# Optimization experiments

Measured on AMD Instinct MI355X. Metric: run time of the kernel, lower is better.

## Reference

```python
import jax, jax.numpy as jnp
import numpy as np

THRESHOLD = 0.7

def _ternize_ste(w, threshold):
    # delta computed without gradient (torch.no_grad in original)
    delta = jax.lax.stop_gradient(threshold * jnp.mean(jnp.abs(w)))
    ternary = jnp.where(w > delta, 1.0, jnp.where(w < -delta, -1.0, 0.0)).astype(w.dtype)
    # STE: forward value = ternary, backward gradient = identity w.r.t. w
    return ternary + (w - jax.lax.stop_gradient(w))

def setup_inputs() -> dict:
    key = jax.random.key(0)
    k1, k2 = jax.random.split(key)
    B, IN, OUT = 32, 4096, 11008
    x = jax.random.normal(k1, (B, IN), dtype=jnp.float32)
    # xavier_uniform init: U(-a, a), a = sqrt(6/(fan_in+fan_out))
    a = float(np.sqrt(6.0 / (IN + OUT)))
    weight = jax.random.uniform(k2, (OUT, IN), dtype=jnp.float32, minval=-a, maxval=a)
    alpha = jnp.ones((1,), dtype=jnp.float32)
    bias = jnp.zeros((OUT,), dtype=jnp.float32)
    return {"x": x, "weight": weight, "alpha": alpha, "bias": bias}

def reference(x, weight, alpha, bias):
    w_ternary = _ternize_ste(weight, THRESHOLD)  # [OUT, IN] values in {-1,0,1}*STE
    # F.linear(x, W*alpha, b) = x @ (W*alpha).T + b
    return jnp.einsum('bi,oi->bo', x, w_ternary * alpha[0]) + bias
```

## Files before the change

### kernel.cpp

```cpp
#include <hip/hip_runtime.h>
#include <hip/hip_bf16.h>

#define OUTN 11008
#define KDIM 4096
#define BDIM 32
#define NT16 688
#define WCOUNT 45088768
#define PF   8
#define NPB  1024

typedef __bf16 bf16x8 __attribute__((ext_vector_type(8)));
typedef float f32x4  __attribute__((ext_vector_type(4)));
typedef float f32x16 __attribute__((ext_vector_type(16)));

__device__ __forceinline__ ushort f2bf(float f) {
    unsigned u = __builtin_bit_cast(unsigned, f);
    u = (u + 0x7FFFu + ((u >> 16) & 1u)) >> 16;
    return (ushort)u;
}

__device__ __forceinline__ unsigned tern1(float w, float d) {
    unsigned b = __builtin_bit_cast(unsigned, w);
    unsigned s = (b & 0x80000000u) | 0x3F800000u;
    return (__builtin_fabsf(w) > d) ? s : 0u;
}
__device__ __forceinline__ unsigned ternpack(float a, float b, float d) {
    return __builtin_amdgcn_perm(tern1(b, d), tern1(a, d), 0x07060302u);
}

__device__ __forceinline__ float delta_fix(double delta_d) {
    float dc = (float)delta_d;
    if ((double)dc > delta_d)
        dc = __builtin_bit_cast(float, __builtin_bit_cast(unsigned, dc) - 1u);
    return dc;
}

__global__ __launch_bounds__(256) void prep_k(const float4* __restrict__ w4,
                                              const float* __restrict__ x,
                                              ushort* __restrict__ xb,
                                              double* __restrict__ dpart) {
    const int tid = blockIdx.x * 256 + threadIdx.x;

    if (threadIdx.x < 32) {
        const int i4 = blockIdx.x * 32 + threadIdx.x;
        const int elem = i4 * 4;
        const int b = elem >> 12;
        const int k = elem & (KDIM - 1);
        const float4 v = ((const float4*)x)[i4];
        ushort4 o;
        o.x = f2bf(v.x); o.y = f2bf(v.y); o.z = f2bf(v.z); o.w = f2bf(v.w);
        *(ushort4*)(xb + ((k >> 3) * 32 + b) * 8 + (k & 7)) = o;
    }

    double s = 0.0;
#pragma unroll 8
    for (int j = 0; j < 43; ++j) {
        float4 v = w4[tid + j * 262144];
        s += (double)(fabsf(v.x) + fabsf(v.y)) + (double)(fabsf(v.z) + fabsf(v.w));
    }
    for (int off = 32; off; off >>= 1) s += __shfl_down(s, off);
    __shared__ double red[4];
    const int lane = threadIdx.x & 63, wv = threadIdx.x >> 6;
    if (lane == 0) red[wv] = s;
    __syncthreads();
    if (threadIdx.x == 0) dpart[blockIdx.x] = red[0] + red[1] + red[2] + red[3];
}

__global__ __launch_bounds__(256, 3) void gemm16_k(const float* __restrict__ W,
                                                   const ushort* __restrict__ xb,
                                                   const double* __restrict__ dpart,
                                                   const float* __restrict__ alpha,
                                                   const float* __restrict__ bias,
                                                   float* __restrict__ out) {
    __shared__ float redf[3][32][16];
    __shared__ double redd[4];
    const int tid = threadIdx.x;
    const int wv = tid >> 6, l = tid & 63;

    {
        double s = 0.0;
#pragma unroll
        for (int j = 0; j < 4; ++j) s += dpart[tid * 4 + j];
        for (int off = 32; off; off >>= 1) s += __shfl_down(s, off);
        if ((tid & 63) == 0) redd[wv] = s;
    }
    __syncthreads();
    const double dsum = redd[0] + redd[1] + redd[2] + redd[3];
    const float delta = delta_fix(0.7 * dsum * (1.0 / (double)WCOUNT));

    const int o0 = blockIdx.x * 16;
    const int kw0 = wv * 1024;
    const int col = l & 15;
    const int kb  = l >> 4;

    const float4* wp = (const float4*)(W + (size_t)(o0 + col) * KDIM + kw0 + kb * 8);
    const uint4* xa0 = (const uint4*)xb + ((size_t)(kw0 >> 3) + kb) * 32 + col;
    const uint4* xa1 = xa0 + 16;

    f32x4 acc0, acc1;
#pragma unroll
    for (int i = 0; i < 4; ++i) { acc0[i] = 0.0f; acc1[i] = 0.0f; }

    float4 Wa[PF], Wb[PF];
    uint4  X0[PF], X1[PF];
#pragma unroll
    for (int p = 0; p < PF; ++p) {
        Wa[p] = wp[p * 8];
        Wb[p] = wp[p * 8 + 1];
        X0[p] = xa0[(size_t)p * 128];
        X1[p] = xa1[(size_t)p * 128];
    }
#pragma unroll
    for (int s = 0; s < 32; ++s) {
        const int bi = s & (PF - 1);
        uint4 bb;
        bb.x = ternpack(Wa[bi].x, Wa[bi].y, delta);
        bb.y = ternpack(Wa[bi].z, Wa[bi].w, delta);
        bb.z = ternpack(Wb[bi].x, Wb[bi].y, delta);
        bb.w = ternpack(Wb[bi].z, Wb[bi].w, delta);
        const bf16x8 bv = __builtin_bit_cast(bf16x8, bb);
        acc0 = __builtin_amdgcn_mfma_f32_16x16x32_bf16(
                   __builtin_bit_cast(bf16x8, X0[bi]), bv, acc0, 0, 0, 0);
        acc1 = __builtin_amdgcn_mfma_f32_16x16x32_bf16(
                   __builtin_bit_cast(bf16x8, X1[bi]), bv, acc1, 0, 0, 0);
        if (s + PF < 32) {
            Wa[bi] = wp[(s + PF) * 8];
            Wb[bi] = wp[(s + PF) * 8 + 1];
            X0[bi] = xa0[(size_t)(s + PF) * 128];
            X1[bi] = xa1[(size_t)(s + PF) * 128];
        }
    }

    if (wv > 0) {
#pragma unroll
        for (int j = 0; j < 4; ++j) {
            redf[wv - 1][kb * 4 + j][col]      = acc0[j];
            redf[wv - 1][16 + kb * 4 + j][col] = acc1[j];
        }
    }
    __syncthreads();
    if (wv == 0) {
        const float a = *alpha;
        const float bn = bias[o0 + col];
#pragma unroll
        for (int j = 0; j < 4; ++j) {
            const int m0 = kb * 4 + j;
            float v0 = acc0[j] + redf[0][m0][col] + redf[1][m0][col] + redf[2][m0][col];
            out[(size_t)m0 * OUTN + o0 + col] = fmaf(a, v0, bn);
            const int m1 = 16 + kb * 4 + j;
            float v1 = acc1[j] + redf[0][m1][col] + redf[1][m1][col] + redf[2][m1][col];
            out[(size_t)m1 * OUTN + o0 + col] = fmaf(a, v1, bn);
        }
    }
}

__global__ __launch_bounds__(256) void abssum_k(const float4* __restrict__ w4,
                                                double* __restrict__ dsum) {
    const int tid = blockIdx.x * 256 + threadIdx.x;
    double s = 0.0;
#pragma unroll 8
    for (int j = 0; j < 43; ++j) {
        float4 v = w4[tid + j * 262144];
        s += (double)(fabsf(v.x) + fabsf(v.y)) + (double)(fabsf(v.z) + fabsf(v.w));
    }
    for (int off = 32; off; off >>= 1) s += __shfl_down(s, off);
    __shared__ double red[4];
    const int lane = threadIdx.x & 63, wv = threadIdx.x >> 6;
    if (lane == 0) red[wv] = s;
    __syncthreads();
    if (threadIdx.x == 0) atomicAdd(dsum, red[0] + red[1] + red[2] + red[3]);
}

__global__ __launch_bounds__(64) void gemm1_k(const float* __restrict__ W,
                                              const float* __restrict__ x,
                                              const double* __restrict__ dsum,
                                              float* __restrict__ dst,
                                              const float* __restrict__ alpha,
                                              const float* __restrict__ bias) {
    const int l = threadIdx.x;
    const int o0 = blockIdx.x * 32;
    const float delta = delta_fix(0.7 * (*dsum) * (1.0 / (double)WCOUNT));
    const int row = l & 31, half = l >> 5;
    const float4* wp = (const float4*)(W + (size_t)(o0 + row) * KDIM + half * 8);
    const float4* xp = (const float4*)(x + (size_t)row * KDIM + half * 8);

    f32x16 acc;
#pragma unroll
    for (int i = 0; i < 16; ++i) acc[i] = 0.0f;

#pragma unroll 8
    for (int s = 0; s < 256; ++s) {
        float4 w0 = wp[s * 4], w1 = wp[s * 4 + 1];
        uint4 bb;
        bb.x = ternpack(w0.x, w0.y, delta);
        bb.y = ternpack(w0.z, w0.w, delta);
        bb.z = ternpack(w1.x, w1.y, delta);
        bb.w = ternpack(w1.z, w1.w, delta);
        float4 v0 = xp[s * 4], v1 = xp[s * 4 + 1];
        struct U { ushort s[8]; } uu;
        uu.s[0] = f2bf(v0.x); uu.s[1] = f2bf(v0.y);
        uu.s[2] = f2bf(v0.z); uu.s[3] = f2bf(v0.w);
        uu.s[4] = f2bf(v1.x); uu.s[5] = f2bf(v1.y);
        uu.s[6] = f2bf(v1.z); uu.s[7] = f2bf(v1.w);
        acc = __builtin_amdgcn_mfma_f32_32x32x16_bf16(
                  __builtin_bit_cast(bf16x8, uu), __builtin_bit_cast(bf16x8, bb),
                  acc, 0, 0, 0);
    }
    const float a = *alpha;
#pragma unroll
    for (int rg = 0; rg < 16; ++rg) {
        const int m = (rg & 3) + 8 * (rg >> 2) + 4 * half;
        const int n = o0 + row;
        dst[(size_t)m * OUTN + n] = fmaf(a, acc[rg], bias[n]);
    }
}

extern "C" void kernel_launch(void* const* d_in, const int* in_sizes, int n_in,
                              void* d_out, int out_size, void* d_ws, size_t ws_size,
                              hipStream_t stream) {
    const float* x     = (const float*)d_in[0];
    const float* W     = (const float*)d_in[1];
    const float* alpha = (const float*)d_in[2];
    const float* bias  = (const float*)d_in[3];
    float* out = (float*)d_out;

    const size_t PART_SZ = (size_t)NPB * 8;
    const size_t XBF_OFF = 65536;
    const size_t XBF_SZ  = (size_t)BDIM * KDIM * 2;

    if (ws_size >= XBF_OFF + XBF_SZ) {
        double* dpart = (double*)d_ws;
        ushort* xb = (ushort*)((char*)d_ws + XBF_OFF);
        prep_k<<<NPB, 256, 0, stream>>>((const float4*)W, x, xb, dpart);
        gemm16_k<<<NT16, 256, 0, stream>>>(W, xb, dpart, alpha, bias, out);
    } else {
        double* dsum = (double*)d_ws;
        (void)hipMemsetAsync(d_ws, 0, 16, stream);
        abssum_k<<<1024, 256, 0, stream>>>((const float4*)W, dsum);
        gemm1_k<<<344, 64, 0, stream>>>(W, x, dsum, out, alpha, bias);
    }
}
```

Measured before the change: 64.31 us.

## Precompute 2-bit ternary weight codes in the abs-sum pass, with a near-threshold exception list

The abs-sum pass that already streams all of W now also writes a 2-bit ternary code per weight. It uses a fixed threshold window placed around the expected delta, and weights inside that window are logged into a per-row exception list through atomics. The GEMM then reads the compact codes instead of re-reading the fp32 weights, which removes the second full pass over W. It fixes the ambiguous entries with a small fp32 correction using a transposed copy of x. If the computed delta falls outside the window, or a row overflows its exception list, it falls back to the original path. The window constants are tuned to the expected weight distribution, and the change adds atomics, extra workspace and a memset.

```diff
diff --git a/kernel.cpp b/kernel.cpp
--- a/kernel.cpp
+++ b/kernel.cpp
@@ -8,6 +8,8 @@
 #define WCOUNT 45088768
 #define PF   8
 #define NPB  1024
+#define DLO  0.0069400f
+#define DHI  0.0070115f
 
 typedef __bf16 bf16x8 __attribute__((ext_vector_type(8)));
 typedef float f32x4  __attribute__((ext_vector_type(4)));
@@ -35,9 +37,21 @@
     return dc;
 }
 
+__device__ __forceinline__ unsigned dec2(unsigned c, int j) {
+    unsigned c0 = (c >> (4 * j)) & 3u;
+    unsigned c1 = (c >> (4 * j + 2)) & 3u;
+    unsigned m = c0 | (c1 << 16);
+    unsigned sel = m + (m << 8) + 0x04000400u;
+    return __builtin_amdgcn_perm(0x00BF3F00u, 0x00808000u, sel);
+}
+
 __global__ __launch_bounds__(256) void prep_k(const float4* __restrict__ w4,
                                               const float* __restrict__ x,
                                               ushort* __restrict__ xb,
+                                              float* __restrict__ xT,
+                                              unsigned char* __restrict__ codes,
+                                              unsigned* __restrict__ cnt,
+                                              uint2* __restrict__ ebuf,
                                               double* __restrict__ dpart) {
     const int tid = blockIdx.x * 256 + threadIdx.x;
 
@@ -50,13 +64,41 @@
         ushort4 o;
         o.x = f2bf(v.x); o.y = f2bf(v.y); o.z = f2bf(v.z); o.w = f2bf(v.w);
         *(ushort4*)(xb + ((k >> 3) * 32 + b) * 8 + (k & 7)) = o;
+        xT[(size_t)(k + 0) * 32 + b] = v.x;
+        xT[(size_t)(k + 1) * 32 + b] = v.y;
+        xT[(size_t)(k + 2) * 32 + b] = v.z;
+        xT[(size_t)(k + 3) * 32 + b] = v.w;
     }
 
     double s = 0.0;
-#pragma unroll 8
+#pragma unroll 4
     for (int j = 0; j < 43; ++j) {
-        float4 v = w4[tid + j * 262144];
-        s += (double)(fabsf(v.x) + fabsf(v.y)) + (double)(fabsf(v.z) + fabsf(v.w));
+        const int i4 = tid + j * 262144;
+        const float4 v = w4[i4];
+        const int row = i4 >> 10;
+        const int kbase = (i4 & 1023) << 2;
+        unsigned cc[4];
+        const float e[4] = {v.x, v.y, v.z, v.w};
+#pragma unroll
+        for (int q = 0; q < 4; ++q) {
+            const float w = e[q];
+            const unsigned wb = __builtin_bit_cast(unsigned, w);
+            const float aw = __builtin_fabsf(w);
+            s += (double)aw;
+            unsigned c;
+            if (aw > DHI) {
+                c = 1u + (wb >> 31);
+            } else if (aw > DLO) {
+                c = 3u;
+                unsigned idx = atomicAdd(&cnt[row], 1u);
+                if (idx < 64u)
+                    ebuf[(size_t)row * 64 + idx] = make_uint2((unsigned)(kbase + q), wb);
+            } else {
+                c = 0u;
+            }
+            cc[q] = c;
+        }
+        codes[i4] = (unsigned char)(cc[0] | (cc[1] << 2) | (cc[2] << 4) | (cc[3] << 6));
     }
     for (int off = 32; off; off >>= 1) s += __shfl_down(s, off);
     __shared__ double red[4];
@@ -67,15 +109,22 @@
 }
 
 __global__ __launch_bounds__(256, 3) void gemm16_k(const float* __restrict__ W,
+                                                   const unsigned char* __restrict__ codes,
                                                    const ushort* __restrict__ xb,
+                                                   const float* __restrict__ xT,
+                                                   const uint2* __restrict__ ebuf,
+                                                   const unsigned* __restrict__ cnt,
                                                    const double* __restrict__ dpart,
                                                    const float* __restrict__ alpha,
                                                    const float* __restrict__ bias,
                                                    float* __restrict__ out) {
     __shared__ float redf[3][32][16];
+    __shared__ float corr[16][33];
     __shared__ double redd[4];
+    __shared__ int sbad;
     const int tid = threadIdx.x;
     const int wv = tid >> 6, l = tid & 63;
+    const int o0 = blockIdx.x * 16;
 
     {
         double s = 0.0;
@@ -84,16 +133,18 @@
         for (int off = 32; off; off >>= 1) s += __shfl_down(s, off);
         if ((tid & 63) == 0) redd[wv] = s;
     }
+    if (tid == 0) sbad = 0;
     __syncthreads();
     const double dsum = redd[0] + redd[1] + redd[2] + redd[3];
-    const float delta = delta_fix(0.7 * dsum * (1.0 / (double)WCOUNT));
-
-    const int o0 = blockIdx.x * 16;
+    const float dc = delta_fix(0.7 * dsum * (1.0 / (double)WCOUNT));
+    if (tid < 16 && cnt[o0 + tid] > 64u) sbad = 1;
+    __syncthreads();
+    const bool ok = (dc >= DLO) && (dc <= DHI) && (sbad == 0);
+
     const int kw0 = wv * 1024;
     const int col = l & 15;
     const int kb  = l >> 4;
 
-    const float4* wp = (const float4*)(W + (size_t)(o0 + col) * KDIM + kw0 + kb * 8);
     const uint4* xa0 = (const uint4*)xb + ((size_t)(kw0 >> 3) + kb) * 32 + col;
     const uint4* xa1 = xa0 + 16;
 
@@ -101,33 +152,49 @@
 #pragma unroll
     for (int i = 0; i < 4; ++i) { acc0[i] = 0.0f; acc1[i] = 0.0f; }
 
-    float4 Wa[PF], Wb[PF];
-    uint4  X0[PF], X1[PF];
-#pragma unroll
-    for (int p = 0; p < PF; ++p) {
-        Wa[p] = wp[p * 8];
-        Wb[p] = wp[p * 8 + 1];
-        X0[p] = xa0[(size_t)p * 128];
-        X1[p] = xa1[(size_t)p * 128];
-    }
-#pragma unroll
-    for (int s = 0; s < 32; ++s) {
-        const int bi = s & (PF - 1);
-        uint4 bb;
-        bb.x = ternpack(Wa[bi].x, Wa[bi].y, delta);
-        bb.y = ternpack(Wa[bi].z, Wa[bi].w, delta);
-        bb.z = ternpack(Wb[bi].x, Wb[bi].y, delta);
-        bb.w = ternpack(Wb[bi].z, Wb[bi].w, delta);
-        const bf16x8 bv = __builtin_bit_cast(bf16x8, bb);
-        acc0 = __builtin_amdgcn_mfma_f32_16x16x32_bf16(
-                   __builtin_bit_cast(bf16x8, X0[bi]), bv, acc0, 0, 0, 0);
-        acc1 = __builtin_amdgcn_mfma_f32_16x16x32_bf16(
-                   __builtin_bit_cast(bf16x8, X1[bi]), bv, acc1, 0, 0, 0);
-        if (s + PF < 32) {
-            Wa[bi] = wp[(s + PF) * 8];
-            Wb[bi] = wp[(s + PF) * 8 + 1];
-            X0[bi] = xa0[(size_t)(s + PF) * 128];
-            X1[bi] = xa1[(size_t)(s + PF) * 128];
+    if (ok) {
+        const ushort* cp = (const ushort*)codes + (size_t)(o0 + col) * 512 + (kw0 >> 3) + kb;
+        unsigned Cc[PF]; uint4 X0[PF], X1[PF];
+#pragma unroll
+        for (int p = 0; p < PF; ++p) {
+            Cc[p] = cp[p * 4];
+            X0[p] = xa0[(size_t)p * 128];
+            X1[p] = xa1[(size_t)p * 128];
+        }
+#pragma unroll
+        for (int s = 0; s < 32; ++s) {
+            const int bi = s & (PF - 1);
+            const unsigned c = Cc[bi];
+            uint4 bb;
+            bb.x = dec2(c, 0); bb.y = dec2(c, 1);
+            bb.z = dec2(c, 2); bb.w = dec2(c, 3);
+            const bf16x8 bv = __builtin_bit_cast(bf16x8, bb);
+            acc0 = __builtin_amdgcn_mfma_f32_16x16x32_bf16(
+                       __builtin_bit_cast(bf16x8, X0[bi]), bv, acc0, 0, 0, 0);
+            acc1 = __builtin_amdgcn_mfma_f32_16x16x32_bf16(
+                       __builtin_bit_cast(bf16x8, X1[bi]), bv, acc1, 0, 0, 0);
+            if (s + PF < 32) {
+                Cc[bi] = cp[(s + PF) * 4];
+                X0[bi] = xa0[(size_t)(s + PF) * 128];
+                X1[bi] = xa1[(size_t)(s + PF) * 128];
+            }
+        }
+    } else {
+        const float4* wp4 = (const float4*)(W + (size_t)(o0 + col) * KDIM + kw0) + kb * 2;
+#pragma unroll 4
+        for (int s = 0; s < 32; ++s) {
+            float4 w0 = wp4[s * 8], w1 = wp4[s * 8 + 1];
+            uint4 bb;
+            bb.x = ternpack(w0.x, w0.y, dc);
+            bb.y = ternpack(w0.z, w0.w, dc);
+            bb.z = ternpack(w1.x, w1.y, dc);
+            bb.w = ternpack(w1.z, w1.w, dc);
+            const bf16x8 bv = __builtin_bit_cast(bf16x8, bb);
+            uint4 a0 = xa0[(size_t)s * 128], a1 = xa1[(size_t)s * 128];
+            acc0 = __builtin_amdgcn_mfma_f32_16x16x32_bf16(
+                       __builtin_bit_cast(bf16x8, a0), bv, acc0, 0, 0, 0);
+            acc1 = __builtin_amdgcn_mfma_f32_16x16x32_bf16(
+                       __builtin_bit_cast(bf16x8, a1), bv, acc1, 0, 0, 0);
         }
     }
 
@@ -138,7 +205,29 @@
             redf[wv - 1][16 + kb * 4 + j][col] = acc1[j];
         }
     }
-    __syncthreads();
+
+    if (ok) {
+        const int m = l & 31;
+        const int h2 = l >> 5;
+#pragma unroll
+        for (int rr = 0; rr < 2; ++rr) {
+            const int r = wv + 4 * (h2 + 2 * rr);
+            const int o = o0 + r;
+            const unsigned n = min(cnt[o], 64u);
+            float rc = 0.0f;
+            for (unsigned e = 0; e < n; ++e) {
+                const uint2 u2 = ebuf[(size_t)o * 64 + e];
+                const float w = __builtin_bit_cast(float, u2.y);
+                if (__builtin_fabsf(w) > dc) {
+                    const float xv = xT[(size_t)u2.x * 32 + m];
+                    rc += (u2.y >> 31) ? -xv : xv;
+                }
+            }
+            corr[r][m] = rc;
+        }
+    }
+    __syncthreads();
+
     if (wv == 0) {
         const float a = *alpha;
         const float bn = bias[o0 + col];
@@ -146,9 +235,11 @@
         for (int j = 0; j < 4; ++j) {
             const int m0 = kb * 4 + j;
             float v0 = acc0[j] + redf[0][m0][col] + redf[1][m0][col] + redf[2][m0][col];
+            if (ok) v0 += corr[col][m0];
             out[(size_t)m0 * OUTN + o0 + col] = fmaf(a, v0, bn);
             const int m1 = 16 + kb * 4 + j;
             float v1 = acc1[j] + redf[0][m1][col] + redf[1][m1][col] + redf[2][m1][col];
+            if (ok) v1 += corr[col][m1];
             out[(size_t)m1 * OUTN + o0 + col] = fmaf(a, v1, bn);
         }
     }
@@ -224,15 +315,24 @@
     const float* bias  = (const float*)d_in[3];
     float* out = (float*)d_out;
 
-    const size_t PART_SZ = (size_t)NPB * 8;
-    const size_t XBF_OFF = 65536;
-    const size_t XBF_SZ  = (size_t)BDIM * KDIM * 2;
-
-    if (ws_size >= XBF_OFF + XBF_SZ) {
+    const size_t CNT_OFF = 8192;
+    const size_t XB_OFF  = 65536;
+    const size_t XT_OFF  = 327680;
+    const size_t EB_OFF  = 1u << 20;
+    const size_t CD_OFF  = 8u << 20;
+    const size_t TOTAL   = CD_OFF + (size_t)(WCOUNT / 4);
+
+    if (ws_size >= TOTAL) {
         double* dpart = (double*)d_ws;
-        ushort* xb = (ushort*)((char*)d_ws + XBF_OFF);
-        prep_k<<<NPB, 256, 0, stream>>>((const float4*)W, x, xb, dpart);
-        gemm16_k<<<NT16, 256, 0, stream>>>(W, xb, dpart, alpha, bias, out);
+        unsigned* cnt = (unsigned*)((char*)d_ws + CNT_OFF);
+        ushort* xb = (ushort*)((char*)d_ws + XB_OFF);
+        float* xT = (float*)((char*)d_ws + XT_OFF);
+        uint2* ebuf = (uint2*)((char*)d_ws + EB_OFF);
+        unsigned char* codes = (unsigned char*)((char*)d_ws + CD_OFF);
+
+        (void)hipMemsetAsync(cnt, 0, OUTN * sizeof(unsigned), stream);
+        prep_k<<<NPB, 256, 0, stream>>>((const float4*)W, x, xb, xT, codes, cnt, ebuf, dpart);
+        gemm16_k<<<NT16, 256, 0, stream>>>(W, codes, xb, xT, ebuf, cnt, dpart, alpha, bias, out);
     } else {
         double* dsum = (double*)d_ws;
         (void)hipMemsetAsync(d_ws, 0, 16, stream);
```

Result: slower. 101.6 us (+57.9%).
